# Kernel optimization log

Measured on AMD Instinct MI355X. Metric: run time of the kernel, lower is better.

Reference implementation:

```python
import jax, jax.numpy as jnp
import numpy as np

B, T, D, H, L = 16, 1024, 1024, 1024, 2


def setup_inputs() -> dict:
    key = jax.random.key(0)
    ks = jax.random.split(key, 7)
    s_ih = float(np.sqrt(6.0 / (4 * H + D)))  # xavier_uniform bound
    s_hh = float(np.sqrt(6.0 / (4 * H + H)))
    return {
        "x": jax.random.normal(ks[0], (B, T, D), dtype=jnp.float32),
        "w_ih0": jax.random.uniform(ks[1], (4 * H, D), jnp.float32, -s_ih, s_ih),
        "w_hh0": jax.random.uniform(ks[2], (4 * H, H), jnp.float32, -s_hh, s_hh),
        "b0": jnp.zeros((4 * H,), jnp.float32),
        "w_ih1": jax.random.uniform(ks[3], (4 * H, H), jnp.float32, -s_ih, s_ih),
        "w_hh1": jax.random.uniform(ks[4], (4 * H, H), jnp.float32, -s_hh, s_hh),
        "b1": jnp.zeros((4 * H,), jnp.float32),
    }


def _cell(x, h, c, w_ih, w_hh, b):
    # gates: [B, 4H]
    gates = x @ w_ih.T + h @ w_hh.T + b
    i, f, g, o = jnp.split(gates, 4, axis=1)
    i = jnp.exp(i)            # exponential input gate (xLSTM sLSTM)
    f = jnp.exp(f)            # exponential forget gate
    g = jnp.tanh(g)
    o = jax.nn.sigmoid(o)
    c = f * c + i * g
    h = o * jnp.tanh(c)
    return h, c


def reference(x, w_ih0, w_hh0, b0, w_ih1, w_hh1, b1):
    b = x.shape[0]
    zeros = jnp.zeros((b, H), x.dtype)
    init = (zeros, zeros, zeros, zeros)  # (h0, c0, h1, c1)

    def step(carry, xt):
        h0, c0, h1, c1 = carry
        h0, c0 = _cell(xt, h0, c0, w_ih0, w_hh0, b0)
        h1, c1 = _cell(h0, h1, c1, w_ih1, w_hh1, b1)
        return (h0, c0, h1, c1), h1

    carry, ys = jax.lax.scan(step, init, jnp.swapaxes(x, 0, 1))  # time-major scan
    out = jnp.swapaxes(ys, 0, 1)  # [B, T, H]
    h0, c0, h1, c1 = carry
    return out, h0, c0, h1, c1
```

## Files before the change

kernel.cpp:

```cpp
#include <hip/hip_runtime.h>
#include <math.h>

namespace {
constexpr int Bt   = 16;
constexpr int Tt   = 1024;
constexpr int Hd   = 1024;
constexpr int NT   = 512;
constexpr int UPB  = 8;
constexpr int NROW = 32;

typedef unsigned long long u64;

__device__ __forceinline__ float sanitize_c(float v) {
  return fminf(fmaxf(v, -3.0e38f), 3.0e38f);
}

template <int CTRL>
__device__ __forceinline__ float dpp_add(float v) {
  int x = __builtin_amdgcn_update_dpp(0, __float_as_int(v), CTRL, 0xF, 0xF, true);
  return v + __int_as_float(x);
}
__device__ __forceinline__ float red8(float v) {
  v = dpp_add<0xB1>(v);
  v = dpp_add<0x4E>(v);
  v = dpp_add<0x141>(v);
  return v;
}

__device__ __forceinline__ u64 ld_h64(const float* p) {
  return __hip_atomic_load((const u64*)p, __ATOMIC_RELAXED, __HIP_MEMORY_SCOPE_AGENT);
}
__device__ __forceinline__ void st_h32(float* p, float v) {
  __hip_atomic_store(p, v, __ATOMIC_RELAXED, __HIP_MEMORY_SCOPE_AGENT);
}
}

__global__ __launch_bounds__(NT)
__attribute__((amdgpu_waves_per_eu(2, 2)))
void slstm_persist(
    const float* __restrict__ x,
    const float* __restrict__ wih0, const float* __restrict__ whh0, const float* __restrict__ b0v,
    const float* __restrict__ wih1, const float* __restrict__ whh1, const float* __restrict__ b1v,
    float* __restrict__ out, float* __restrict__ ws)
{
  __shared__ __align__(16) float in0[Bt * Hd];
  __shared__ __align__(16) float in1[Bt * Hd];
  __shared__ __align__(16) float red[64 * 17 * 4];
  __shared__ float gatel[NROW * Bt];
  __shared__ float cst[UPB * Bt];
  __shared__ float biasl[NROW];

  const int tid  = threadIdx.x;
  const int bid  = blockIdx.x;
  const int w    = tid >> 6;
  const int lane = tid & 63;
  const int kslo = lane & 7;
  const int rg   = lane >> 3;
  const int ks   = w * 8 + kslo;
  const bool isB = ks >= 32;
  const int ksl  = ks & 31;
  const int cell = bid >> 7;
  const int blk  = bid & 127;
  const int ubase = blk * UPB;

  unsigned* flags = (unsigned*)ws;
  float* h0buf = ws + 1024;
  float* h1buf = h0buf + 2 * Bt * Hd;

  const float* wmat = (cell == 0) ? (isB ? whh0 : wih0) : (isB ? whh1 : wih1);
  const float* bv   = (cell == 0) ? b0v : b1v;

  const int ro0 = ((0 + kslo) & 7) * 16;
  const int ro1 = ((1 + kslo) & 7) * 16;
  const int ro2 = ((2 + kslo) & 7) * 16;
  const int ro3 = ((3 + kslo) & 7) * 16;
  const int ro4 = ((4 + kslo) & 7) * 16;
  const int ro5 = ((5 + kslo) & 7) * 16;
  const int ro6 = ((6 + kslo) & 7) * 16;
  const int ro7 = ((7 + kslo) & 7) * 16;

  float4 w00,w01,w02,w03,w04,w05,w06,w07;
  float4 w10,w11,w12,w13,w14,w15,w16,w17;
  float4 w20,w21,w22,w23,w24,w25,w26,w27;
  float4 w30,w31,w32,w33,w34,w35,w36,w37;
#define LDW(r) { \
    const int lr = rg * 4 + r; \
    const char* wb = (const char*)(wmat + (size_t)((lr >> 3) * Hd + ubase + (lr & 7)) * Hd + ksl * 32); \
    w##r##0 = *(const float4*)(wb + ro0); w##r##1 = *(const float4*)(wb + ro1); \
    w##r##2 = *(const float4*)(wb + ro2); w##r##3 = *(const float4*)(wb + ro3); \
    w##r##4 = *(const float4*)(wb + ro4); w##r##5 = *(const float4*)(wb + ro5); \
    w##r##6 = *(const float4*)(wb + ro6); w##r##7 = *(const float4*)(wb + ro7); }
  LDW(0) LDW(1) LDW(2) LDW(3)
#undef LDW

  if (tid < NROW) biasl[tid] = bv[(tid >> 3) * Hd + ubase + (tid & 7)];
  if (tid < UPB * Bt) cst[tid] = 0.f;
  __syncthreads();

  unsigned gen = 0;

  for (int k = 0; k <= Tt; ++k) {
    const bool active = (cell == 0) ? (k < Tt) : (k >= 1);
    if (active) {
      if (cell == 0) {
        const float* xs = x + (size_t)k * Hd;
        #pragma unroll
        for (int p = 0; p < 8; ++p) {
          const int e = p * 2048 + tid * 4;
          const int b = e >> 10, d = e & 1023;
          *(float4*)(in0 + e) = *(const float4*)(xs + (size_t)b * (Tt * Hd) + d);
        }
        if (k > 0) {
          const float* hs = h0buf + ((k - 1) & 1) * (Bt * Hd);
          #pragma unroll
          for (int p = 0; p < 8; ++p) {
            const int e = p * 2048 + tid * 4;
            u64 lo = ld_h64(hs + e);
            u64 hi = ld_h64(hs + e + 2);
            ((u64*)(in1 + e))[0] = lo;
            ((u64*)(in1 + e))[1] = hi;
          }
        } else {
          #pragma unroll
          for (int p = 0; p < 8; ++p)
            *(float4*)(in1 + p * 2048 + tid * 4) = make_float4(0.f, 0.f, 0.f, 0.f);
        }
      } else {
        const float* hs = h0buf + ((k - 1) & 1) * (Bt * Hd);
        #pragma unroll
        for (int p = 0; p < 8; ++p) {
          const int e = p * 2048 + tid * 4;
          u64 lo = ld_h64(hs + e);
          u64 hi = ld_h64(hs + e + 2);
          ((u64*)(in0 + e))[0] = lo;
          ((u64*)(in0 + e))[1] = hi;
        }
        if (k >= 2) {
          const float* hs1 = h1buf + (k & 1) * (Bt * Hd);
          #pragma unroll
          for (int p = 0; p < 8; ++p) {
            const int e = p * 2048 + tid * 4;
            u64 lo = ld_h64(hs1 + e);
            u64 hi = ld_h64(hs1 + e + 2);
            ((u64*)(in1 + e))[0] = lo;
            ((u64*)(in1 + e))[1] = hi;
          }
        } else {
          #pragma unroll
          for (int p = 0; p < 8; ++p)
            *(float4*)(in1 + p * 2048 + tid * 4) = make_float4(0.f, 0.f, 0.f, 0.f);
        }
      }
      __syncthreads();

      const float* myin = (isB ? in1 : in0) + ksl * 32;
      #pragma unroll 2
      for (int b = 0; b < Bt; ++b) {
        const char* pb = (const char*)(myin + b * Hd);
        float a0 = 0.f, a1 = 0.f, a2 = 0.f, a3 = 0.f;
#define STEPC(c) { const float4 v = *(const float4*)(pb + ro##c); \
        a0 = fmaf(v.x, w0##c.x, a0); a0 = fmaf(v.y, w0##c.y, a0); \
        a0 = fmaf(v.z, w0##c.z, a0); a0 = fmaf(v.w, w0##c.w, a0); \
        a1 = fmaf(v.x, w1##c.x, a1); a1 = fmaf(v.y, w1##c.y, a1); \
        a1 = fmaf(v.z, w1##c.z, a1); a1 = fmaf(v.w, w1##c.w, a1); \
        a2 = fmaf(v.x, w2##c.x, a2); a2 = fmaf(v.y, w2##c.y, a2); \
        a2 = fmaf(v.z, w2##c.z, a2); a2 = fmaf(v.w, w2##c.w, a2); \
        a3 = fmaf(v.x, w3##c.x, a3); a3 = fmaf(v.y, w3##c.y, a3); \
        a3 = fmaf(v.z, w3##c.z, a3); a3 = fmaf(v.w, w3##c.w, a3); }
        STEPC(0) STEPC(1) STEPC(2) STEPC(3)
        STEPC(4) STEPC(5) STEPC(6) STEPC(7)
#undef STEPC
        a0 = red8(a0); a1 = red8(a1); a2 = red8(a2); a3 = red8(a3);
        if (kslo == 0)
          *(float4*)&red[((w * 8 + rg) * 17 + b) * 4] = make_float4(a0, a1, a2, a3);
      }
      __syncthreads();

      {
        const int rg2 = tid >> 6, rem = tid & 63, b2 = rem >> 2, r2 = rem & 3;
        float s = 0.f;
        #pragma unroll
        for (int ww = 0; ww < 8; ++ww)
          s += red[((ww * 8 + rg2) * 17 + b2) * 4 + r2];
        const int lr = rg2 * 4 + r2;
        gatel[lr * Bt + b2] = s + biasl[lr];
      }
      __syncthreads();

      if (tid < UPB * Bt) {
        const int u = tid >> 4, b2 = tid & 15;
        const float gi = gatel[(0 * UPB + u) * Bt + b2];
        const float gf = gatel[(1 * UPB + u) * Bt + b2];
        const float gg = gatel[(2 * UPB + u) * Bt + b2];
        const float go = gatel[(3 * UPB + u) * Bt + b2];
        const float ig = expf(gi);
        const float fg = expf(gf);
        const float g_ = tanhf(gg);
        const float og = 1.f / (1.f + expf(-go));
        const float cn = fg * cst[tid] + ig * g_;
        cst[tid] = cn;
        const float h = og * tanhf(cn);
        const int j = ubase + u;
        const size_t fin = (size_t)Bt * Tt * Hd;
        if (cell == 0) {
          st_h32(&h0buf[(k & 1) * (Bt * Hd) + b2 * Hd + j], h);
          if (k == Tt - 1) {
            out[fin + b2 * Hd + j] = h;
            out[fin + Bt * Hd + b2 * Hd + j] = sanitize_c(cn);
          }
        } else {
          const int t = k - 1;
          out[((size_t)b2 * Tt + t) * Hd + j] = h;
          st_h32(&h1buf[(t & 1) * (Bt * Hd) + b2 * Hd + j], h);
          if (t == Tt - 1) {
            out[fin + 2 * Bt * Hd + b2 * Hd + j] = h;
            out[fin + 3 * Bt * Hd + b2 * Hd + j] = sanitize_c(cn);
          }
        }
      }
    }

    ++gen;
    asm volatile("s_waitcnt vmcnt(0)" ::: "memory");
    __syncthreads();
    if (tid == 0)
      __hip_atomic_store(&flags[bid], gen, __ATOMIC_RELAXED, __HIP_MEMORY_SCOPE_AGENT);
    if (tid < 256)
      while (__hip_atomic_load(&flags[tid], __ATOMIC_RELAXED, __HIP_MEMORY_SCOPE_AGENT) < gen)
        __builtin_amdgcn_s_sleep(1);
    asm volatile("" ::: "memory");
    __syncthreads();
  }
}

extern "C" void kernel_launch(void* const* d_in, const int* in_sizes, int n_in,
                              void* d_out, int out_size, void* d_ws, size_t ws_size,
                              hipStream_t stream) {
  (void)hipMemsetAsync(d_ws, 0, 4096, stream);

  const float* x    = (const float*)d_in[0];
  const float* wih0 = (const float*)d_in[1];
  const float* whh0 = (const float*)d_in[2];
  const float* b0   = (const float*)d_in[3];
  const float* wih1 = (const float*)d_in[4];
  const float* whh1 = (const float*)d_in[5];
  const float* b1   = (const float*)d_in[6];

  slstm_persist<<<256, NT, 0, stream>>>(x, wih0, whh0, b0, wih1, whh1, b1,
                                        (float*)d_out, (float*)d_ws);
}
```

Baseline: 17.59 ms.

## Overlap input-side matmul with grid-barrier wait and skew layer-1 pipeline

Splits each block's waves into two roles. The first four waves compute the input-projection half of the gate matmul, for which x is prefetched one step ahead and h0 comes from a triple-buffered ring. Meanwhile the other four waves spin on the per-block flags and then load the recurrent state. Layer 1 is skewed by an extra step, and output writes are moved after the flag publish so they leave the critical path. The aim is to hide the grid-barrier latency behind useful compute. The cost is a more intricate buffer-indexing and synchronisation scheme, which raises the risk of races.

New measurement: 16.88 ms. -4.0%, faster.

```diff
diff --git a/kernel.cpp b/kernel.cpp
--- a/kernel.cpp
+++ b/kernel.cpp
@@ -65,7 +65,7 @@
 
   unsigned* flags = (unsigned*)ws;
   float* h0buf = ws + 1024;
-  float* h1buf = h0buf + 2 * Bt * Hd;
+  float* h1buf = h0buf + 3 * Bt * Hd;
 
   const float* wmat = (cell == 0) ? (isB ? whh0 : wih0) : (isB ? whh1 : wih1);
   const float* bv   = (cell == 0) ? b0v : b1v;
@@ -95,69 +95,17 @@
 
   if (tid < NROW) biasl[tid] = bv[(tid >> 3) * Hd + ubase + (tid & 7)];
   if (tid < UPB * Bt) cst[tid] = 0.f;
+
+  if (cell == 0) {
+    #pragma unroll
+    for (int p = 0; p < 8; ++p) {
+      const int e = p * 2048 + tid * 4;
+      const int b = e >> 10, d = e & 1023;
+      *(float4*)(in0 + e) = *(const float4*)(x + (size_t)b * (Tt * Hd) + d);
+    }
+  }
   __syncthreads();
 
-  unsigned gen = 0;
-
-  for (int k = 0; k <= Tt; ++k) {
-    const bool active = (cell == 0) ? (k < Tt) : (k >= 1);
-    if (active) {
-      if (cell == 0) {
-        const float* xs = x + (size_t)k * Hd;
-        #pragma unroll
-        for (int p = 0; p < 8; ++p) {
-          const int e = p * 2048 + tid * 4;
-          const int b = e >> 10, d = e & 1023;
-          *(float4*)(in0 + e) = *(const float4*)(xs + (size_t)b * (Tt * Hd) + d);
-        }
-        if (k > 0) {
-          const float* hs = h0buf + ((k - 1) & 1) * (Bt * Hd);
-          #pragma unroll
-          for (int p = 0; p < 8; ++p) {
-            const int e = p * 2048 + tid * 4;
-            u64 lo = ld_h64(hs + e);
-            u64 hi = ld_h64(hs + e + 2);
-            ((u64*)(in1 + e))[0] = lo;
-            ((u64*)(in1 + e))[1] = hi;
-          }
-        } else {
-          #pragma unroll
-          for (int p = 0; p < 8; ++p)
-            *(float4*)(in1 + p * 2048 + tid * 4) = make_float4(0.f, 0.f, 0.f, 0.f);
-        }
-      } else {
-        const float* hs = h0buf + ((k - 1) & 1) * (Bt * Hd);
-        #pragma unroll
-        for (int p = 0; p < 8; ++p) {
-          const int e = p * 2048 + tid * 4;
-          u64 lo = ld_h64(hs + e);
-          u64 hi = ld_h64(hs + e + 2);
-          ((u64*)(in0 + e))[0] = lo;
-          ((u64*)(in0 + e))[1] = hi;
-        }
-        if (k >= 2) {
-          const float* hs1 = h1buf + (k & 1) * (Bt * Hd);
-          #pragma unroll
-          for (int p = 0; p < 8; ++p) {
-            const int e = p * 2048 + tid * 4;
-            u64 lo = ld_h64(hs1 + e);
-            u64 hi = ld_h64(hs1 + e + 2);
-            ((u64*)(in1 + e))[0] = lo;
-            ((u64*)(in1 + e))[1] = hi;
-          }
-        } else {
-          #pragma unroll
-          for (int p = 0; p < 8; ++p)
-            *(float4*)(in1 + p * 2048 + tid * 4) = make_float4(0.f, 0.f, 0.f, 0.f);
-        }
-      }
-      __syncthreads();
-
-      const float* myin = (isB ? in1 : in0) + ksl * 32;
-      #pragma unroll 2
-      for (int b = 0; b < Bt; ++b) {
-        const char* pb = (const char*)(myin + b * Hd);
-        float a0 = 0.f, a1 = 0.f, a2 = 0.f, a3 = 0.f;
 #define STEPC(c) { const float4 v = *(const float4*)(pb + ro##c); \
         a0 = fmaf(v.x, w0##c.x, a0); a0 = fmaf(v.y, w0##c.y, a0); \
         a0 = fmaf(v.z, w0##c.z, a0); a0 = fmaf(v.w, w0##c.w, a0); \
@@ -167,23 +115,89 @@
         a2 = fmaf(v.z, w2##c.z, a2); a2 = fmaf(v.w, w2##c.w, a2); \
         a3 = fmaf(v.x, w3##c.x, a3); a3 = fmaf(v.y, w3##c.y, a3); \
         a3 = fmaf(v.z, w3##c.z, a3); a3 = fmaf(v.w, w3##c.w, a3); }
-        STEPC(0) STEPC(1) STEPC(2) STEPC(3)
-        STEPC(4) STEPC(5) STEPC(6) STEPC(7)
-#undef STEPC
-        a0 = red8(a0); a1 = red8(a1); a2 = red8(a2); a3 = red8(a3);
-        if (kslo == 0)
-          *(float4*)&red[((w * 8 + rg) * 17 + b) * 4] = make_float4(a0, a1, a2, a3);
-      }
+#define MATMUL(INBUF) { \
+    const float* myin = (INBUF) + ksl * 32; \
+    _Pragma("unroll 2") \
+    for (int b = 0; b < Bt; ++b) { \
+      const char* pb = (const char*)(myin + b * Hd); \
+      float a0 = 0.f, a1 = 0.f, a2 = 0.f, a3 = 0.f; \
+      STEPC(0) STEPC(1) STEPC(2) STEPC(3) \
+      STEPC(4) STEPC(5) STEPC(6) STEPC(7) \
+      a0 = red8(a0); a1 = red8(a1); a2 = red8(a2); a3 = red8(a3); \
+      if (kslo == 0) \
+        *(float4*)&red[((w * 8 + rg) * 17 + b) * 4] = make_float4(a0, a1, a2, a3); \
+    } }
+
+  for (int k = 0; k <= Tt + 1; ++k) {
+    const bool act = (cell == 0) ? (k < Tt) : (k >= 2);
+
+    if (w < 4) {
+      if (act) { MATMUL(in0) }
+    } else {
+      const unsigned tgt = (unsigned)k;
+      const int f = tid - 256;
+      while (__hip_atomic_load(&flags[f], __ATOMIC_RELAXED, __HIP_MEMORY_SCOPE_AGENT) < tgt)
+        __builtin_amdgcn_s_sleep(1);
+    }
+    __syncthreads();
+
+    if (w >= 4) {
+      if (act) {
+        const int s = tid - 256;
+        if ((cell == 0 && k == 0) || (cell == 1 && k == 2)) {
+          #pragma unroll
+          for (int p = 0; p < 16; ++p)
+            *(float4*)(in1 + p * 1024 + s * 4) = make_float4(0.f, 0.f, 0.f, 0.f);
+        } else {
+          const float* src = (cell == 0) ? (h0buf + ((k - 1) % 3) * (Bt * Hd))
+                                         : (h1buf + ((k - 1) & 1) * (Bt * Hd));
+          #pragma unroll
+          for (int p = 0; p < 16; ++p) {
+            const int e = p * 1024 + s * 4;
+            u64 lo = ld_h64(src + e), hi = ld_h64(src + e + 2);
+            ((u64*)(in1 + e))[0] = lo;
+            ((u64*)(in1 + e))[1] = hi;
+          }
+        }
+      }
+    } else {
+      const int s = tid;
+      if (cell == 0) {
+        if (k + 1 < Tt) {
+          #pragma unroll
+          for (int p = 0; p < 16; ++p) {
+            const int e = p * 1024 + s * 4;
+            const int b = e >> 10, d = e & 1023;
+            *(float4*)(in0 + e) =
+                *(const float4*)(x + (size_t)b * (Tt * Hd) + (size_t)(k + 1) * Hd + d);
+          }
+        }
+      } else if (k >= 1 && k <= Tt) {
+        const float* src = h0buf + ((k - 1) % 3) * (Bt * Hd);
+        #pragma unroll 8
+        for (int p = 0; p < 16; ++p) {
+          const int e = p * 1024 + s * 4;
+          u64 lo = ld_h64(src + e), hi = ld_h64(src + e + 2);
+          ((u64*)(in0 + e))[0] = lo;
+          ((u64*)(in0 + e))[1] = hi;
+        }
+      }
+    }
+    __syncthreads();
+
+    float oh = 0.f, oc = 0.f;
+    if (act) {
+      if (w >= 4) { MATMUL(in1) }
       __syncthreads();
 
       {
         const int rg2 = tid >> 6, rem = tid & 63, b2 = rem >> 2, r2 = rem & 3;
-        float s = 0.f;
+        float sgm = 0.f;
         #pragma unroll
         for (int ww = 0; ww < 8; ++ww)
-          s += red[((ww * 8 + rg2) * 17 + b2) * 4 + r2];
+          sgm += red[((ww * 8 + rg2) * 17 + b2) * 4 + r2];
         const int lr = rg2 * 4 + r2;
-        gatel[lr * Bt + b2] = s + biasl[lr];
+        gatel[lr * Bt + b2] = sgm + biasl[lr];
       }
       __syncthreads();
 
@@ -200,37 +214,42 @@
         const float cn = fg * cst[tid] + ig * g_;
         cst[tid] = cn;
         const float h = og * tanhf(cn);
+        oh = h; oc = cn;
         const int j = ubase + u;
-        const size_t fin = (size_t)Bt * Tt * Hd;
         if (cell == 0) {
-          st_h32(&h0buf[(k & 1) * (Bt * Hd) + b2 * Hd + j], h);
-          if (k == Tt - 1) {
-            out[fin + b2 * Hd + j] = h;
-            out[fin + Bt * Hd + b2 * Hd + j] = sanitize_c(cn);
-          }
+          st_h32(&h0buf[(k % 3) * (Bt * Hd) + b2 * Hd + j], h);
         } else {
-          const int t = k - 1;
-          out[((size_t)b2 * Tt + t) * Hd + j] = h;
-          st_h32(&h1buf[(t & 1) * (Bt * Hd) + b2 * Hd + j], h);
-          if (t == Tt - 1) {
-            out[fin + 2 * Bt * Hd + b2 * Hd + j] = h;
-            out[fin + 3 * Bt * Hd + b2 * Hd + j] = sanitize_c(cn);
-          }
-        }
-      }
-    }
-
-    ++gen;
+          st_h32(&h1buf[(k & 1) * (Bt * Hd) + b2 * Hd + j], h);
+        }
+      }
+    }
+
     asm volatile("s_waitcnt vmcnt(0)" ::: "memory");
     __syncthreads();
     if (tid == 0)
-      __hip_atomic_store(&flags[bid], gen, __ATOMIC_RELAXED, __HIP_MEMORY_SCOPE_AGENT);
-    if (tid < 256)
-      while (__hip_atomic_load(&flags[tid], __ATOMIC_RELAXED, __HIP_MEMORY_SCOPE_AGENT) < gen)
-        __builtin_amdgcn_s_sleep(1);
-    asm volatile("" ::: "memory");
-    __syncthreads();
+      __hip_atomic_store(&flags[bid], (unsigned)(k + 1), __ATOMIC_RELAXED, __HIP_MEMORY_SCOPE_AGENT);
+
+    if (act && tid < UPB * Bt) {
+      const int u = tid >> 4, b2 = tid & 15, j = ubase + u;
+      const size_t fin = (size_t)Bt * Tt * Hd;
+      if (cell == 0) {
+        if (k == Tt - 1) {
+          out[fin + b2 * Hd + j] = oh;
+          out[fin + Bt * Hd + b2 * Hd + j] = sanitize_c(oc);
+        }
+      } else {
+        const int t = k - 2;
+        out[((size_t)b2 * Tt + t) * Hd + j] = oh;
+        if (t == Tt - 1) {
+          out[fin + 2 * Bt * Hd + b2 * Hd + j] = oh;
+          out[fin + 3 * Bt * Hd + b2 * Hd + j] = sanitize_c(oc);
+        }
+      }
+    }
   }
+  asm volatile("s_waitcnt vmcnt(0)" ::: "memory");
+#undef MATMUL
+#undef STEPC
 }
 
 extern "C" void kernel_launch(void* const* d_in, const int* in_sizes, int n_in,
```
